# Kernel tuning notes

Measured on AMD Instinct MI355X. Metric: run time of the kernel, lower is better.

## Reference

```python
import jax, jax.numpy as jnp
import numpy as np

B, T, CM, CZ, H = 2, 512, 256, 128, 16
DH = CM // H  # 16
EPS = 1e-5


def setup_inputs() -> dict:
    root = jax.random.key(0)
    ks = jax.random.split(root, 16)
    n = lambda i, shape: jax.random.normal(ks[i], shape, dtype=jnp.float32)
    s = np.float32(1.0 / np.sqrt(CM))
    return dict(
        query=n(0, (B, T, CM)),
        key=n(1, (B, T, CM)),
        value=n(2, (B, T, CM)),
        pos_embedding=n(3, (B, 2 * T - 1, CM)),  # T2 = 2T-1 relative positions
        z=n(4, (B, T, T, CZ)),
        mask=jax.random.randint(ks[5], (B, 1, T), 0, 2) > 0,
        Wq=n(6, (CM, CM)) * s, bq=jnp.zeros((CM,), jnp.float32),
        Wk=n(7, (CM, CM)) * s, bk=jnp.zeros((CM,), jnp.float32),
        Wv=n(8, (CM, CM)) * s, bv=jnp.zeros((CM,), jnp.float32),
        Wp=n(9, (CM, CM)) * s,
        u_bias=n(10, (H, DH)) * np.float32(0.1),
        v_bias=n(11, (H, DH)) * np.float32(0.1),
        Wo=n(12, (CM, CM)) * s, bo=jnp.zeros((CM,), jnp.float32),
        ln_g=jnp.ones((CZ,), jnp.float32), ln_b=jnp.zeros((CZ,), jnp.float32),
        Wz=n(13, (CZ, H)) * np.float32(1.0 / np.sqrt(CZ)),
    )


def _relative_shift(ps):
    # ps: (B, H, T1, T2) -> Transformer-XL relative shift, keep first T2//2+1 cols
    b, h, t1, t2 = ps.shape
    padded = jnp.pad(ps, ((0, 0), (0, 0), (0, 0), (1, 0)))  # (b,h,t1,t2+1)
    padded = padded.reshape(b, h, t2 + 1, t1)
    shifted = padded[:, :, 1:, :].reshape(b, h, t1, t2)
    return shifted[..., : t2 // 2 + 1]


def reference(query, key, value, pos_embedding, z, mask,
              Wq, bq, Wk, bk, Wv, bv, Wp, u_bias, v_bias, Wo, bo,
              ln_g, ln_b, Wz):
    b = query.shape[0]
    q = (query @ Wq.T + bq).reshape(b, -1, H, DH)          # (b,T,H,dh)
    k = (key @ Wk.T + bk).reshape(b, -1, H, DH)
    v = (value @ Wv.T + bv).reshape(b, -1, H, DH)
    p = (pos_embedding @ Wp.T).reshape(b, -1, H, DH)       # (b,2T-1,H,dh)

    content = jnp.einsum('bihd,bjhd->bhij', q + u_bias, k)     # (b,H,T,T)
    pos = jnp.einsum('bihd,bjhd->bhij', q + v_bias, p)         # (b,H,T,2T-1)
    pos = _relative_shift(pos)                                  # (b,H,T,T)

    # z bias: LayerNorm over c_z then project to heads (chunking in torch is a no-op math-wise)
    mu = jnp.mean(z, axis=-1, keepdims=True)
    var = jnp.var(z, axis=-1, keepdims=True)
    zn = (z - mu) * jax.lax.rsqrt(var + EPS) * ln_g + ln_b
    z_bias = jnp.einsum('bijc,ch->bhij', zn, Wz)                # (b,H,T,T)

    score = (content + pos) / np.float32(np.sqrt(DH)) + z_bias
    score = jnp.where(mask[:, None, :, :], jnp.float32(-10000.0), score)
    attn = jax.nn.softmax(score, axis=-1)  # dropout is identity in eval

    ctx = jnp.einsum('bhij,bjhd->bihd', attn, v).reshape(b, -1, CM)
    return ctx @ Wo.T + bo
```

## Files before the change

### kernel.cpp

```cpp
#include <hip/hip_runtime.h>
#include <hip/hip_bf16.h>

typedef __attribute__((ext_vector_type(8))) short short8;
typedef __attribute__((ext_vector_type(4))) short short4v;
typedef __attribute__((ext_vector_type(4))) float f32x4;

#define LD4(dst, v4) { dst[0]=(v4).x; dst[1]=(v4).y; dst[2]=(v4).z; dst[3]=(v4).w; }

static __device__ __forceinline__ short f2bf(float f) {
    union { float f; unsigned u; } v; v.f = f;
    unsigned r = (v.u + 0x7FFFu + ((v.u >> 16) & 1u)) >> 16;
    return (short)r;
}
static __device__ __forceinline__ float bf2f(short s) {
    union { unsigned u; float f; } v; v.u = ((unsigned)(unsigned short)s) << 16;
    return v.f;
}
static __device__ __forceinline__ unsigned cvt_pk_bf16(float lo, float hi) {
    unsigned r;
    asm volatile("v_cvt_pk_bf16_f32 %0, %1, %2" : "=v"(r) : "v"(lo), "v"(hi));
    return r;
}

static __device__ __forceinline__ void proj_tile(
    const float* __restrict__ X, const float* __restrict__ W,
    const float* __restrict__ bias, float* __restrict__ Yf,
    short* __restrict__ Yb, int M, int base, float* xs)
{
    int rt = base >> 1, ct = base & 1;
    int t = threadIdx.x;
    int row_base = rt * 32;
    {
        int r = t >> 3, k0 = (t & 7) * 32;
        int row = row_base + r;
        if (row < M) {
            const float* xp = X + (size_t)row * 256 + k0;
            #pragma unroll
            for (int q = 0; q < 8; ++q) {
                float4 v = *(const float4*)(xp + q * 4);
                xs[(k0 + q * 4 + 0) * 36 + r] = v.x;
                xs[(k0 + q * 4 + 1) * 36 + r] = v.y;
                xs[(k0 + q * 4 + 2) * 36 + r] = v.z;
                xs[(k0 + q * 4 + 3) * 36 + r] = v.w;
            }
        } else {
            #pragma unroll
            for (int q = 0; q < 32; ++q) xs[(k0 + q) * 36 + r] = 0.f;
        }
    }
    __syncthreads();
    int c_base = ct * 128 + (t & 31) * 4;
    int r_base = (t >> 5) * 4;
    float acc[4][4];
    #pragma unroll
    for (int a = 0; a < 4; ++a)
        #pragma unroll
        for (int b = 0; b < 4; ++b) acc[a][b] = 0.f;
    for (int k = 0; k < 256; k += 4) {
        float w0[4], w1[4], w2[4], w3[4];
        { float4 v = *(const float4*)(W + (size_t)(c_base + 0) * 256 + k); LD4(w0, v); }
        { float4 v = *(const float4*)(W + (size_t)(c_base + 1) * 256 + k); LD4(w1, v); }
        { float4 v = *(const float4*)(W + (size_t)(c_base + 2) * 256 + k); LD4(w2, v); }
        { float4 v = *(const float4*)(W + (size_t)(c_base + 3) * 256 + k); LD4(w3, v); }
        #pragma unroll
        for (int kk = 0; kk < 4; ++kk) {
            float xl[4];
            float4 xv = *(const float4*)(&xs[(k + kk) * 36 + r_base]);
            LD4(xl, xv);
            #pragma unroll
            for (int ri = 0; ri < 4; ++ri) {
                acc[ri][0] += xl[ri] * w0[kk];
                acc[ri][1] += xl[ri] * w1[kk];
                acc[ri][2] += xl[ri] * w2[kk];
                acc[ri][3] += xl[ri] * w3[kk];
            }
        }
    }
    #pragma unroll
    for (int ri = 0; ri < 4; ++ri) {
        int row = row_base + r_base + ri;
        if (row < M) {
            float o0 = acc[ri][0] + (bias ? bias[c_base + 0] : 0.f);
            float o1 = acc[ri][1] + (bias ? bias[c_base + 1] : 0.f);
            float o2 = acc[ri][2] + (bias ? bias[c_base + 2] : 0.f);
            float o3 = acc[ri][3] + (bias ? bias[c_base + 3] : 0.f);
            if (Yb) {
                short4v o; o[0] = f2bf(o0); o[1] = f2bf(o1); o[2] = f2bf(o2); o[3] = f2bf(o3);
                *(short4v*)(Yb + (size_t)row * 256 + c_base) = o;
            } else {
                float4 o; o.x = o0; o.y = o1; o.z = o2; o.w = o3;
                *(float4*)(Yf + (size_t)row * 256 + c_base) = o;
            }
        }
    }
}

__global__ void k_proj(const float* __restrict__ query, const float* __restrict__ key,
                       const float* __restrict__ value, const float* __restrict__ pos,
                       const float* __restrict__ Wq, const float* __restrict__ bq,
                       const float* __restrict__ Wk, const float* __restrict__ bk,
                       const float* __restrict__ Wv, const float* __restrict__ bv,
                       const float* __restrict__ Wp,
                       const float* __restrict__ ln_g, const float* __restrict__ ln_b,
                       const float* __restrict__ Wz, const int* __restrict__ mask,
                       float* __restrict__ qb, short* __restrict__ kbf,
                       short* __restrict__ vbf, short* __restrict__ pbf,
                       short* __restrict__ wzp, float* __restrict__ Ah, float* __restrict__ Ch,
                       int* __restrict__ idx, int* __restrict__ cnt)
{
    __shared__ float xs[256 * 36];
    int bx = blockIdx.x;
    if (bx == 320) {
        int lane = threadIdx.x & 63, wave = threadIdx.x >> 6;
        if (wave == 0) {
            for (int b = 0; b < 2; ++b) {
                int* idxb = idx + b * 512;
                #pragma unroll
                for (int q = 0; q < 8; ++q) idxb[q * 64 + lane] = -1;
                int total = 0;
                for (int q = 0; q < 8; ++q) {
                    int j = q * 64 + lane;
                    int u = (mask[b * 512 + j] == 0) ? 1 : 0;
                    unsigned long long bal = __ballot(u);
                    int p = total + __popcll(bal & ((1ull << lane) - 1ull));
                    if (u) idxb[p] = j;
                    total += (int)__popcll(bal);
                }
                if (total == 0) {
                    for (int q = 0; q < 8; ++q) idxb[q * 64 + lane] = q * 64 + lane;
                    total = 512;
                }
                if (lane == 0) cnt[b] = total;
            }
        } else if (wave == 1) {
            for (int id = lane; id < 2048; id += 64) {
                int m = id >> 9, rem = id & 511, l = rem >> 3, ii = rem & 7;
                int c = m * 32 + ((l >> 4) << 3) + ii, h = l & 15;
                wzp[id] = f2bf(ln_g[c] * Wz[c * 16 + h]);
            }
        } else if (wave == 2) {
            int h = lane & 15, part = lane >> 4;
            float a = 0.f, c = 0.f;
            #pragma unroll 4
            for (int cc = part * 32; cc < part * 32 + 32; ++cc) {
                float wv = Wz[cc * 16 + h];
                a += ln_g[cc] * wv;
                c += ln_b[cc] * wv;
            }
            a += __shfl_xor(a, 16); a += __shfl_xor(a, 32);
            c += __shfl_xor(c, 16); c += __shfl_xor(c, 32);
            if (part == 0) { Ah[h] = a; Ch[h] = c; }
        }
        return;
    }
    if (bx < 64)       proj_tile(query, Wq, bq, qb, nullptr, 1024, bx, xs);
    else if (bx < 128) proj_tile(key,   Wk, bk, nullptr, kbf, 1024, bx - 64, xs);
    else if (bx < 192) proj_tile(value, Wv, bv, nullptr, vbf, 1024, bx - 128, xs);
    else               proj_tile(pos,   Wp, nullptr, nullptr, pbf, 2046, bx - 192, xs);
}

__global__ void __launch_bounds__(256, 4) k_z(
    const float* __restrict__ z, const short* __restrict__ wzp,
    const float* __restrict__ Ah, const float* __restrict__ Ch,
    const int* __restrict__ idx, const int* __restrict__ cnt,
    const short* __restrict__ kbf, const short* __restrict__ vbf,
    short* __restrict__ kbfC, short* __restrict__ vbTC, short* __restrict__ zacc)
{
    __shared__ short ldsb[8448];
    int bx = blockIdx.x;
    const short8 z8v = {0,0,0,0,0,0,0,0};
    if (bx < 32) {
        short* st = ldsb;
        int b = bx >> 4, jn0 = (bx & 15) * 32;
        int t = threadIdx.x;
        int r = t >> 3, cc = (t & 7) * 32;
        int jn = jn0 + r;
        int jv = idx[b * 512 + jn];
        {
            short* dst = kbfC + ((size_t)b * 512 + jn) * 256 + cc;
            if (jv >= 0) {
                const short* src = kbf + ((size_t)b * 512 + jv) * 256 + cc;
                #pragma unroll
                for (int q = 0; q < 4; ++q) *(short8*)(dst + q * 8) = *(const short8*)(src + q * 8);
            } else {
                #pragma unroll
                for (int q = 0; q < 4; ++q) *(short8*)(dst + q * 8) = z8v;
            }
        }
        {
            if (jv >= 0) {
                const short* src = vbf + ((size_t)b * 512 + jv) * 256 + cc;
                #pragma unroll
                for (int q = 0; q < 4; ++q) *(short8*)(&st[r * 264 + cc + q * 8]) = *(const short8*)(src + q * 8);
            } else {
                #pragma unroll
                for (int q = 0; q < 4; ++q) *(short8*)(&st[r * 264 + cc + q * 8]) = z8v;
            }
            __syncthreads();
            int c = t;
            short tmp[32];
            #pragma unroll
            for (int q = 0; q < 32; ++q) tmp[q] = st[q * 264 + c];
            short* dst = vbTC + ((size_t)b * 256 + c) * 512 + jn0;
            #pragma unroll
            for (int q = 0; q < 4; ++q) *(short8*)(dst + q * 8) = *(const short8*)(&tmp[q * 8]);
        }
        return;
    }
    int wave = threadIdx.x >> 6, lane = threadIdx.x & 63;
    int w = (bx - 32) * 4 + wave;
    int bi = w >> 5, tl = w & 31;
    int b = bi >> 9;
    int np = (min(cnt[b], 512) + 31) & ~31;
    if (tl * 16 >= np) return;
    short* zs = ldsb + wave * 2112;
    const int* idxr = idx + b * 512 + tl * 16;
    const float* zb_ = z + (size_t)bi * 65536;
    int l5 = lane >> 5, l31 = lane & 31;
    int idxv = idxr[lane & 15];
    #pragma unroll
    for (int m = 0; m < 8; ++m) {
        int r = 2 * m + l5;
        int jv = __shfl(idxv, r);
        int jr = (jv < 0) ? 0 : jv;
        float4 v = *(const float4*)(zb_ + (size_t)jr * 128 + l31 * 4);
        uint2 pk;
        pk.x = cvt_pk_bf16(v.x, v.y);
        pk.y = cvt_pk_bf16(v.z, v.w);
        *(uint2*)(&zs[r * 132 + l31 * 4]) = pk;
    }
    int h = lane & 15, g = lane >> 4;
    short8 wz[4];
    #pragma unroll
    for (int m = 0; m < 4; ++m) wz[m] = *(const short8*)(wzp + m * 512 + lane * 8);
    short8 af[4];
    float sum = 0.f, sq = 0.f;
    #pragma unroll
    for (int m = 0; m < 4; ++m) {
        short4v a0 = *(const short4v*)(&zs[h * 132 + g * 8 + m * 32]);
        short4v a1 = *(const short4v*)(&zs[h * 132 + g * 8 + m * 32 + 4]);
        short8 s8;
        s8[0] = a0[0]; s8[1] = a0[1]; s8[2] = a0[2]; s8[3] = a0[3];
        s8[4] = a1[0]; s8[5] = a1[1]; s8[6] = a1[2]; s8[7] = a1[3];
        af[m] = s8;
        #pragma unroll
        for (int ii = 0; ii < 8; ++ii) {
            float x = bf2f(s8[ii]);
            sum += x;
            sq = fmaf(x, x, sq);
        }
    }
    sum += __shfl_xor(sum, 16); sum += __shfl_xor(sum, 32);
    sq  += __shfl_xor(sq, 16);  sq  += __shfl_xor(sq, 32);
    float mu = sum * (1.f / 128.f);
    float rs = rsqrtf(sq * (1.f / 128.f) - mu * mu + 1e-5f);
    f32x4 acc = {0.f, 0.f, 0.f, 0.f};
    #pragma unroll
    for (int m = 0; m < 4; ++m)
        acc = __builtin_amdgcn_mfma_f32_16x16x32_bf16(af[m], wz[m], acc, 0, 0, 0);
    float ah = Ah[h], ch = Ch[h];
    short4v o;
    #pragma unroll
    for (int reg = 0; reg < 4; ++reg) {
        int orow = g * 4 + reg;
        float mo = __shfl(mu, orow);
        float ro = __shfl(rs, orow);
        o[reg] = f2bf(ro * (acc[reg] - mo * ah) + ch);
    }
    *(short4v*)(zacc + ((size_t)bi * 16 + h) * 512 + tl * 16 + g * 4) = o;
}

__global__ void __launch_bounds__(256, 4) k_attn4(
    const float* __restrict__ qb, const short* __restrict__ kbfC, const short* __restrict__ pbf,
    const short* __restrict__ zacc,
    const float* __restrict__ u_bias, const float* __restrict__ v_bias,
    const int* __restrict__ idx, const int* __restrict__ cnt,
    const short* __restrict__ vbTC,
    const float* __restrict__ Wo, const float* __restrict__ bo, float* __restrict__ out)
{
    __shared__ short wT[16 * 520];
    __shared__ float redm[64], reds[64];
    __shared__ float ctx_lds[256];
    const short8 zero8 = {0, 0, 0, 0, 0, 0, 0, 0};

    int bi = blockIdx.x;
    int b = bi >> 9, i = bi & 511;
    int t = threadIdx.x;
    int lane = t & 63, wave = t >> 6;
    int h = lane & 15, g = lane >> 4;
    int np = (min(cnt[b], 512) + 31) & ~31;
    int nt16 = np >> 4;

    bool act = ((h & 1) == (g >> 1));
    int m_act = act ? (h >> 1) : 8;
    short8 qu8 = zero8, qv8 = zero8;
    {
        int c0q = h * 16 + (g & 1) * 8;
        const float* qp = qb + (size_t)bi * 256 + c0q;
        #pragma unroll
        for (int ii = 0; ii < 8; ++ii) {
            float qv_ = qp[ii];
            qu8[ii] = f2bf(0.25f * (qv_ + u_bias[c0q + ii]));
            qv8[ii] = f2bf(0.25f * (qv_ + v_bias[c0q + ii]));
        }
        if (!act) { qu8 = zero8; qv8 = zero8; }
    }

    f32x4 sc[8];
    float mloc = -3.0e38f;
    #pragma unroll
    for (int q = 0; q < 8; ++q) {
        int tl = wave + q * 4;
        if (tl < nt16) {
            int jn = tl * 16 + h;
            int jvh = idx[b * 512 + jn];
            int jrp = 511 + ((jvh < 0) ? 0 : jvh) - i;
            const short* kr = kbfC + ((size_t)b * 512 + jn) * 256 + g * 8;
            const short* pr = pbf + ((size_t)b * 1023 + jrp) * 256 + g * 8;
            f32x4 acp = {0.f, 0.f, 0.f, 0.f};
            #pragma unroll
            for (int m = 0; m < 8; ++m) {
                short8 ka = *(const short8*)(kr + m * 32);
                short8 pa = *(const short8*)(pr + m * 32);
                short8 bu = (m == m_act) ? qu8 : zero8;
                short8 bv = (m == m_act) ? qv8 : zero8;
                acp = __builtin_amdgcn_mfma_f32_16x16x32_bf16(ka, bu, acp, 0, 0, 0);
                acp = __builtin_amdgcn_mfma_f32_16x16x32_bf16(pa, bv, acp, 0, 0, 0);
            }
            short4v za = *(const short4v*)(zacc + ((size_t)bi * 16 + h) * 512 + tl * 16 + g * 4);
            int4 jv4 = *(const int4*)(idx + b * 512 + tl * 16 + g * 4);
            int jj4[4]; jj4[0] = jv4.x; jj4[1] = jv4.y; jj4[2] = jv4.z; jj4[3] = jv4.w;
            #pragma unroll
            for (int reg = 0; reg < 4; ++reg) {
                float s = acp[reg] + bf2f(za[reg]);
                s = (jj4[reg] < 0) ? -3.0e38f : s;
                sc[q][reg] = s;
                mloc = fmaxf(mloc, s);
            }
        }
    }

    mloc = fmaxf(mloc, __shfl_xor(mloc, 16));
    mloc = fmaxf(mloc, __shfl_xor(mloc, 32));
    redm[wave * 16 + h] = mloc;
    __syncthreads();
    float mg = fmaxf(fmaxf(redm[h], redm[16 + h]), fmaxf(redm[32 + h], redm[48 + h]));
    float ssum = 0.f;
    #pragma unroll
    for (int q = 0; q < 8; ++q) {
        int tl = wave + q * 4;
        if (tl < nt16) {
            #pragma unroll
            for (int reg = 0; reg < 4; ++reg) {
                float e = __expf(sc[q][reg] - mg);
                sc[q][reg] = e;
                ssum += e;
            }
        }
    }
    ssum += __shfl_xor(ssum, 16); ssum += __shfl_xor(ssum, 32);
    reds[wave * 16 + h] = ssum;
    __syncthreads();
    float sg = reds[h] + reds[16 + h] + reds[32 + h] + reds[48 + h];
    float inv = 1.f / sg;
    #pragma unroll
    for (int q = 0; q < 8; ++q) {
        int tl = wave + q * 4;
        if (tl < nt16) {
            short4v w4;
            #pragma unroll
            for (int reg = 0; reg < 4; ++reg) w4[reg] = f2bf(sc[q][reg] * inv);
            *(short4v*)(&wT[h * 520 + tl * 16 + g * 4]) = w4;
        }
    }
    __syncthreads();

    #pragma unroll
    for (int q = 0; q < 4; ++q) {
        int hp = wave * 4 + q;
        int c0 = hp * 16;
        const short* vrow = vbTC + ((size_t)b * 256 + c0 + h) * 512;
        f32x4 a0 = {0.f, 0.f, 0.f, 0.f};
        for (int jn0 = 0; jn0 < np; jn0 += 32) {
            short8 wA = *(const short8*)(&wT[hp * 520 + jn0 + g * 8]);
            short8 vB = *(const short8*)(vrow + jn0 + g * 8);
            a0 = __builtin_amdgcn_mfma_f32_16x16x32_bf16(wA, vB, a0, 0, 0, 0);
        }
        if (g == 0) ctx_lds[c0 + h] = a0[0];
    }
    __syncthreads();

    {
        float acc = bo[t];
        const float* wrow = Wo + (size_t)t * 256;
        #pragma unroll 4
        for (int k = 0; k < 256; k += 8) {
            float4 w0 = *(const float4*)(wrow + k);
            float4 w1 = *(const float4*)(wrow + k + 4);
            acc += ctx_lds[k + 0] * w0.x + ctx_lds[k + 1] * w0.y
                 + ctx_lds[k + 2] * w0.z + ctx_lds[k + 3] * w0.w
                 + ctx_lds[k + 4] * w1.x + ctx_lds[k + 5] * w1.y
                 + ctx_lds[k + 6] * w1.z + ctx_lds[k + 7] * w1.w;
        }
        out[(size_t)bi * 256 + t] = acc;
    }
}

extern "C" void kernel_launch(void* const* d_in, const int* in_sizes, int n_in,
                              void* d_out, int out_size, void* d_ws, size_t ws_size,
                              hipStream_t stream) {
    const float* query = (const float*)d_in[0];
    const float* key   = (const float*)d_in[1];
    const float* value = (const float*)d_in[2];
    const float* pos   = (const float*)d_in[3];
    const float* z     = (const float*)d_in[4];
    const int*   mask  = (const int*)d_in[5];
    const float* Wq = (const float*)d_in[6];
    const float* bq = (const float*)d_in[7];
    const float* Wk = (const float*)d_in[8];
    const float* bk = (const float*)d_in[9];
    const float* Wv = (const float*)d_in[10];
    const float* bv = (const float*)d_in[11];
    const float* Wp = (const float*)d_in[12];
    const float* u_bias = (const float*)d_in[13];
    const float* v_bias = (const float*)d_in[14];
    const float* Wo = (const float*)d_in[15];
    const float* bo = (const float*)d_in[16];
    const float* ln_g = (const float*)d_in[17];
    const float* ln_b = (const float*)d_in[18];
    const float* Wz = (const float*)d_in[19];

    char* ws = (char*)d_ws;
    float* qb   = (float*)(ws + 0);
    short* kbf  = (short*)(ws + (1u << 20));
    short* vbf  = (short*)(ws + 1572864u);
    short* pbf  = (short*)(ws + (2u << 20));
    short* wzp  = (short*)(ws + (3u << 20));
    float* Ah   = (float*)(ws + (3u << 20) + 4096);
    float* Ch   = (float*)(ws + (3u << 20) + 4160);
    int*   idx  = (int*)(ws + (3u << 20) + 8192);
    int*   cnt  = (int*)(ws + (3u << 20) + 16384);
    short* kbfC = (short*)(ws + (4u << 20));
    short* vbTC = (short*)(ws + 4718592u);
    short* zacc = (short*)(ws + (5u << 20));

    hipLaunchKernelGGL(k_proj, dim3(321), dim3(256), 0, stream,
                       query, key, value, pos, Wq, bq, Wk, bk, Wv, bv, Wp,
                       ln_g, ln_b, Wz, mask,
                       qb, kbf, vbf, pbf, wzp, Ah, Ch, idx, cnt);
    hipLaunchKernelGGL(k_z, dim3(8224), dim3(256), 0, stream,
                       z, wzp, Ah, Ch, idx, cnt, kbf, vbf, kbfC, vbTC, zacc);
    hipLaunchKernelGGL(k_attn4, dim3(1024), dim3(256), 0, stream,
                       qb, kbfC, pbf, zacc, u_bias, v_bias, idx, cnt, vbTC,
                       Wo, bo, (float*)d_out);
}
```

Before: 183.9 us.

## Fuse projection, z-bias and attention kernels into one persistent grid-barrier megakernel

Replaces the three separate launches (projection, z LayerNorm/gather, attention) with one persistent kernel of 1024 blocks. The stages are separated by software grid barriers built on atomic counters, which a small init kernel resets. It also adds a first stage that transposes Wq/Wk/Wv/Wp/Wo into workspace so the projection and output GEMVs read weights with coalesced row access, and the projection is retiled into 16-row tiles. The aim is to remove inter-kernel launch gaps and tails and to improve weight access. The cost is extra barrier and transpose work and a dependence on all 1024 blocks being co-resident, with a spin timeout that could silently break correctness.

```diff
diff --git a/kernel.cpp b/kernel.cpp
--- a/kernel.cpp
+++ b/kernel.cpp
@@ -5,7 +5,7 @@
 typedef __attribute__((ext_vector_type(4))) short short4v;
 typedef __attribute__((ext_vector_type(4))) float f32x4;
 
-#define LD4(dst, v4) { dst[0]=(v4).x; dst[1]=(v4).y; dst[2]=(v4).z; dst[3]=(v4).w; }
+#define NBLK 1024
 
 static __device__ __forceinline__ short f2bf(float f) {
     union { float f; unsigned u; } v; v.f = f;
@@ -22,96 +22,75 @@
     return r;
 }
 
-static __device__ __forceinline__ void proj_tile(
-    const float* __restrict__ X, const float* __restrict__ W,
-    const float* __restrict__ bias, float* __restrict__ Yf,
-    short* __restrict__ Yb, int M, int base, float* xs)
-{
-    int rt = base >> 1, ct = base & 1;
-    int t = threadIdx.x;
-    int row_base = rt * 32;
-    {
-        int r = t >> 3, k0 = (t & 7) * 32;
-        int row = row_base + r;
-        if (row < M) {
-            const float* xp = X + (size_t)row * 256 + k0;
-            #pragma unroll
-            for (int q = 0; q < 8; ++q) {
-                float4 v = *(const float4*)(xp + q * 4);
-                xs[(k0 + q * 4 + 0) * 36 + r] = v.x;
-                xs[(k0 + q * 4 + 1) * 36 + r] = v.y;
-                xs[(k0 + q * 4 + 2) * 36 + r] = v.z;
-                xs[(k0 + q * 4 + 3) * 36 + r] = v.w;
-            }
+__global__ void k_init(int* bar) { if (threadIdx.x < 16) bar[threadIdx.x] = 0; }
+
+static __device__ __forceinline__ void grid_barrier(int* bar, int idx) {
+    __syncthreads();
+    if (threadIdx.x == 0) {
+        __threadfence();
+        int old = __hip_atomic_fetch_add(&bar[idx * 2], 1, __ATOMIC_ACQ_REL, __HIP_MEMORY_SCOPE_AGENT);
+        if (old == NBLK - 1) {
+            __hip_atomic_store(&bar[idx * 2 + 1], 1, __ATOMIC_RELEASE, __HIP_MEMORY_SCOPE_AGENT);
         } else {
-            #pragma unroll
-            for (int q = 0; q < 32; ++q) xs[(k0 + q) * 36 + r] = 0.f;
-        }
+            int spins = 0;
+            while (__hip_atomic_load(&bar[idx * 2 + 1], __ATOMIC_ACQUIRE, __HIP_MEMORY_SCOPE_AGENT) == 0) {
+                __builtin_amdgcn_s_sleep(2);
+                if (++spins > (1 << 22)) break;
+            }
+        }
+        __threadfence();
     }
     __syncthreads();
-    int c_base = ct * 128 + (t & 31) * 4;
-    int r_base = (t >> 5) * 4;
-    float acc[4][4];
-    #pragma unroll
-    for (int a = 0; a < 4; ++a)
-        #pragma unroll
-        for (int b = 0; b < 4; ++b) acc[a][b] = 0.f;
-    for (int k = 0; k < 256; k += 4) {
-        float w0[4], w1[4], w2[4], w3[4];
-        { float4 v = *(const float4*)(W + (size_t)(c_base + 0) * 256 + k); LD4(w0, v); }
-        { float4 v = *(const float4*)(W + (size_t)(c_base + 1) * 256 + k); LD4(w1, v); }
-        { float4 v = *(const float4*)(W + (size_t)(c_base + 2) * 256 + k); LD4(w2, v); }
-        { float4 v = *(const float4*)(W + (size_t)(c_base + 3) * 256 + k); LD4(w3, v); }
-        #pragma unroll
-        for (int kk = 0; kk < 4; ++kk) {
-            float xl[4];
-            float4 xv = *(const float4*)(&xs[(k + kk) * 36 + r_base]);
-            LD4(xl, xv);
-            #pragma unroll
-            for (int ri = 0; ri < 4; ++ri) {
-                acc[ri][0] += xl[ri] * w0[kk];
-                acc[ri][1] += xl[ri] * w1[kk];
-                acc[ri][2] += xl[ri] * w2[kk];
-                acc[ri][3] += xl[ri] * w3[kk];
-            }
-        }
-    }
-    #pragma unroll
-    for (int ri = 0; ri < 4; ++ri) {
-        int row = row_base + r_base + ri;
-        if (row < M) {
-            float o0 = acc[ri][0] + (bias ? bias[c_base + 0] : 0.f);
-            float o1 = acc[ri][1] + (bias ? bias[c_base + 1] : 0.f);
-            float o2 = acc[ri][2] + (bias ? bias[c_base + 2] : 0.f);
-            float o3 = acc[ri][3] + (bias ? bias[c_base + 3] : 0.f);
-            if (Yb) {
-                short4v o; o[0] = f2bf(o0); o[1] = f2bf(o1); o[2] = f2bf(o2); o[3] = f2bf(o3);
-                *(short4v*)(Yb + (size_t)row * 256 + c_base) = o;
-            } else {
-                float4 o; o.x = o0; o.y = o1; o.z = o2; o.w = o3;
-                *(float4*)(Yf + (size_t)row * 256 + c_base) = o;
-            }
-        }
-    }
-}
-
-__global__ void k_proj(const float* __restrict__ query, const float* __restrict__ key,
-                       const float* __restrict__ value, const float* __restrict__ pos,
-                       const float* __restrict__ Wq, const float* __restrict__ bq,
-                       const float* __restrict__ Wk, const float* __restrict__ bk,
-                       const float* __restrict__ Wv, const float* __restrict__ bv,
-                       const float* __restrict__ Wp,
-                       const float* __restrict__ ln_g, const float* __restrict__ ln_b,
-                       const float* __restrict__ Wz, const int* __restrict__ mask,
-                       float* __restrict__ qb, short* __restrict__ kbf,
-                       short* __restrict__ vbf, short* __restrict__ pbf,
-                       short* __restrict__ wzp, float* __restrict__ Ah, float* __restrict__ Ch,
-                       int* __restrict__ idx, int* __restrict__ cnt)
+}
+
+__global__ void __launch_bounds__(256, 4) k_mega(
+    const float* __restrict__ query, const float* __restrict__ key,
+    const float* __restrict__ value, const float* __restrict__ pos,
+    const float* __restrict__ z, const int* __restrict__ mask,
+    const float* __restrict__ Wq, const float* __restrict__ bq,
+    const float* __restrict__ Wk, const float* __restrict__ bk,
+    const float* __restrict__ Wv, const float* __restrict__ bv,
+    const float* __restrict__ Wp, const float* __restrict__ u_bias,
+    const float* __restrict__ v_bias, const float* __restrict__ Wo,
+    const float* __restrict__ bo, const float* __restrict__ ln_g,
+    const float* __restrict__ ln_b, const float* __restrict__ Wz,
+    float* __restrict__ qb, short* __restrict__ kbf, short* __restrict__ vbf,
+    short* __restrict__ pbf, short* __restrict__ wzp,
+    float* __restrict__ Ah, float* __restrict__ Ch,
+    int* __restrict__ idx, int* __restrict__ cnt, int* __restrict__ bar,
+    short* __restrict__ kbfC, short* __restrict__ vbTC, short* __restrict__ zacc,
+    float* __restrict__ WqT, float* __restrict__ WkT, float* __restrict__ WvT,
+    float* __restrict__ WpT, float* __restrict__ WoT, float* __restrict__ out)
 {
-    __shared__ float xs[256 * 36];
-    int bx = blockIdx.x;
-    if (bx == 320) {
-        int lane = threadIdx.x & 63, wave = threadIdx.x >> 6;
+    __shared__ __align__(16) char lds_raw[36864];
+    int bx = blockIdx.x, t = threadIdx.x;
+    int lane = t & 63, wave = t >> 6;
+
+    if (bx < 80) {
+        int mat = bx >> 4, tile = bx & 15, rt = tile >> 2, ct = tile & 3;
+        const float* src = (mat == 0) ? Wq : (mat == 1) ? Wk : (mat == 2) ? Wv : (mat == 3) ? Wp : Wo;
+        float* dst = (mat == 0) ? WqT : (mat == 1) ? WkT : (mat == 2) ? WvT : (mat == 3) ? WpT : WoT;
+        float* xsf = (float*)lds_raw;
+        int r = t >> 2, c0 = (t & 3) * 16;
+        const float* sp = src + (size_t)(rt * 64 + r) * 256 + ct * 64 + c0;
+        #pragma unroll
+        for (int u = 0; u < 4; ++u) {
+            float4 v = *(const float4*)(sp + u * 4);
+            xsf[r * 69 + c0 + u * 4 + 0] = v.x; xsf[r * 69 + c0 + u * 4 + 1] = v.y;
+            xsf[r * 69 + c0 + u * 4 + 2] = v.z; xsf[r * 69 + c0 + u * 4 + 3] = v.w;
+        }
+        __syncthreads();
+        float* dp = dst + (size_t)(ct * 64 + r) * 256 + rt * 64 + c0;
+        #pragma unroll
+        for (int u = 0; u < 4; ++u) {
+            float4 o;
+            o.x = xsf[(c0 + u * 4 + 0) * 69 + r];
+            o.y = xsf[(c0 + u * 4 + 1) * 69 + r];
+            o.z = xsf[(c0 + u * 4 + 2) * 69 + r];
+            o.w = xsf[(c0 + u * 4 + 3) * 69 + r];
+            *(float4*)(dp + u * 4) = o;
+        }
+    } else if (bx == 1023) {
         if (wave == 0) {
             for (int b = 0; b < 2; ++b) {
                 int* idxb = idx + b * 512;
@@ -151,258 +130,291 @@
             c += __shfl_xor(c, 16); c += __shfl_xor(c, 32);
             if (part == 0) { Ah[h] = a; Ch[h] = c; }
         }
-        return;
     }
-    if (bx < 64)       proj_tile(query, Wq, bq, qb, nullptr, 1024, bx, xs);
-    else if (bx < 128) proj_tile(key,   Wk, bk, nullptr, kbf, 1024, bx - 64, xs);
-    else if (bx < 192) proj_tile(value, Wv, bv, nullptr, vbf, 1024, bx - 128, xs);
-    else               proj_tile(pos,   Wp, nullptr, nullptr, pbf, 2046, bx - 192, xs);
-}
-
-__global__ void __launch_bounds__(256, 4) k_z(
-    const float* __restrict__ z, const short* __restrict__ wzp,
-    const float* __restrict__ Ah, const float* __restrict__ Ch,
-    const int* __restrict__ idx, const int* __restrict__ cnt,
-    const short* __restrict__ kbf, const short* __restrict__ vbf,
-    short* __restrict__ kbfC, short* __restrict__ vbTC, short* __restrict__ zacc)
-{
-    __shared__ short ldsb[8448];
-    int bx = blockIdx.x;
-    const short8 z8v = {0,0,0,0,0,0,0,0};
-    if (bx < 32) {
-        short* st = ldsb;
-        int b = bx >> 4, jn0 = (bx & 15) * 32;
-        int t = threadIdx.x;
-        int r = t >> 3, cc = (t & 7) * 32;
-        int jn = jn0 + r;
-        int jv = idx[b * 512 + jn];
+    grid_barrier(bar, 0);
+
+    if (bx < 640) {
+        const float* X; const float* WT_; const float* bias;
+        float* Yf = nullptr; short* Yb = nullptr; int M; int tile;
+        if (bx < 128)      { X = query; WT_ = WqT; bias = bq;      Yf = qb;  M = 1024; tile = bx; }
+        else if (bx < 256) { X = key;   WT_ = WkT; bias = bk;      Yb = kbf; M = 1024; tile = bx - 128; }
+        else if (bx < 384) { X = value; WT_ = WvT; bias = bv;      Yb = vbf; M = 1024; tile = bx - 256; }
+        else               { X = pos;   WT_ = WpT; bias = nullptr; Yb = pbf; M = 2046; tile = bx - 384; }
+        float* xs = (float*)lds_raw;
+        int rt = tile >> 1, ctile = tile & 1, row_base = rt * 16;
         {
-            short* dst = kbfC + ((size_t)b * 512 + jn) * 256 + cc;
-            if (jv >= 0) {
-                const short* src = kbf + ((size_t)b * 512 + jv) * 256 + cc;
-                #pragma unroll
-                for (int q = 0; q < 4; ++q) *(short8*)(dst + q * 8) = *(const short8*)(src + q * 8);
+            int r = t & 15, kq = (t >> 4) * 16;
+            int row = row_base + r;
+            if (row < M) {
+                const float* xp = X + (size_t)row * 256 + kq;
+                #pragma unroll
+                for (int u = 0; u < 4; ++u) {
+                    float4 v = *(const float4*)(xp + u * 4);
+                    xs[(kq + u * 4 + 0) * 17 + r] = v.x;
+                    xs[(kq + u * 4 + 1) * 17 + r] = v.y;
+                    xs[(kq + u * 4 + 2) * 17 + r] = v.z;
+                    xs[(kq + u * 4 + 3) * 17 + r] = v.w;
+                }
             } else {
                 #pragma unroll
-                for (int q = 0; q < 4; ++q) *(short8*)(dst + q * 8) = z8v;
-            }
-        }
-        {
-            if (jv >= 0) {
-                const short* src = vbf + ((size_t)b * 512 + jv) * 256 + cc;
-                #pragma unroll
-                for (int q = 0; q < 4; ++q) *(short8*)(&st[r * 264 + cc + q * 8]) = *(const short8*)(src + q * 8);
-            } else {
-                #pragma unroll
-                for (int q = 0; q < 4; ++q) *(short8*)(&st[r * 264 + cc + q * 8]) = z8v;
+                for (int u = 0; u < 16; ++u) xs[(kq + u) * 17 + r] = 0.f;
+            }
+        }
+        __syncthreads();
+        int cb = ctile * 128 + (t & 31) * 4;
+        int rb = (t >> 5) * 2;
+        float acc[2][4] = {{0.f,0.f,0.f,0.f},{0.f,0.f,0.f,0.f}};
+        for (int k = 0; k < 256; ++k) {
+            float4 w = *(const float4*)(WT_ + (size_t)k * 256 + cb);
+            float x0 = xs[k * 17 + rb], x1 = xs[k * 17 + rb + 1];
+            acc[0][0] += x0 * w.x; acc[0][1] += x0 * w.y;
+            acc[0][2] += x0 * w.z; acc[0][3] += x0 * w.w;
+            acc[1][0] += x1 * w.x; acc[1][1] += x1 * w.y;
+            acc[1][2] += x1 * w.z; acc[1][3] += x1 * w.w;
+        }
+        #pragma unroll
+        for (int ri = 0; ri < 2; ++ri) {
+            int row = row_base + rb + ri;
+            if (row < M) {
+                float o0 = acc[ri][0] + (bias ? bias[cb + 0] : 0.f);
+                float o1 = acc[ri][1] + (bias ? bias[cb + 1] : 0.f);
+                float o2 = acc[ri][2] + (bias ? bias[cb + 2] : 0.f);
+                float o3 = acc[ri][3] + (bias ? bias[cb + 3] : 0.f);
+                if (Yb) {
+                    short4v o; o[0] = f2bf(o0); o[1] = f2bf(o1); o[2] = f2bf(o2); o[3] = f2bf(o3);
+                    *(short4v*)(Yb + (size_t)row * 256 + cb) = o;
+                } else {
+                    float4 o; o.x = o0; o.y = o1; o.z = o2; o.w = o3;
+                    *(float4*)(Yf + (size_t)row * 256 + cb) = o;
+                }
+            }
+        }
+    }
+    grid_barrier(bar, 1);
+
+    {
+        const short8 z8v = {0,0,0,0,0,0,0,0};
+        if (bx < 32) {
+            short* st = (short*)lds_raw;
+            int b = bx >> 4, jn0 = (bx & 15) * 32;
+            int r = t >> 3, cc = (t & 7) * 32;
+            int jn = jn0 + r;
+            int jv = idx[b * 512 + jn];
+            {
+                short* dst = kbfC + ((size_t)b * 512 + jn) * 256 + cc;
+                if (jv >= 0) {
+                    const short* src = kbf + ((size_t)b * 512 + jv) * 256 + cc;
+                    #pragma unroll
+                    for (int q = 0; q < 4; ++q) *(short8*)(dst + q * 8) = *(const short8*)(src + q * 8);
+                } else {
+                    #pragma unroll
+                    for (int q = 0; q < 4; ++q) *(short8*)(dst + q * 8) = z8v;
+                }
+            }
+            {
+                if (jv >= 0) {
+                    const short* src = vbf + ((size_t)b * 512 + jv) * 256 + cc;
+                    #pragma unroll
+                    for (int q = 0; q < 4; ++q) *(short8*)(&st[r * 264 + cc + q * 8]) = *(const short8*)(src + q * 8);
+                } else {
+                    #pragma unroll
+                    for (int q = 0; q < 4; ++q) *(short8*)(&st[r * 264 + cc + q * 8]) = z8v;
+                }
+                __syncthreads();
+                int c = t;
+                short tmp[32];
+                #pragma unroll
+                for (int q = 0; q < 32; ++q) tmp[q] = st[q * 264 + c];
+                short* dst = vbTC + ((size_t)b * 256 + c) * 512 + jn0;
+                #pragma unroll
+                for (int q = 0; q < 4; ++q) *(short8*)(dst + q * 8) = *(const short8*)(&tmp[q * 8]);
             }
             __syncthreads();
-            int c = t;
-            short tmp[32];
-            #pragma unroll
-            for (int q = 0; q < 32; ++q) tmp[q] = st[q * 264 + c];
-            short* dst = vbTC + ((size_t)b * 256 + c) * 512 + jn0;
-            #pragma unroll
-            for (int q = 0; q < 4; ++q) *(short8*)(dst + q * 8) = *(const short8*)(&tmp[q * 8]);
-        }
-        return;
-    }
-    int wave = threadIdx.x >> 6, lane = threadIdx.x & 63;
-    int w = (bx - 32) * 4 + wave;
-    int bi = w >> 5, tl = w & 31;
-    int b = bi >> 9;
-    int np = (min(cnt[b], 512) + 31) & ~31;
-    if (tl * 16 >= np) return;
-    short* zs = ldsb + wave * 2112;
-    const int* idxr = idx + b * 512 + tl * 16;
-    const float* zb_ = z + (size_t)bi * 65536;
-    int l5 = lane >> 5, l31 = lane & 31;
-    int idxv = idxr[lane & 15];
-    #pragma unroll
-    for (int m = 0; m < 8; ++m) {
-        int r = 2 * m + l5;
-        int jv = __shfl(idxv, r);
-        int jr = (jv < 0) ? 0 : jv;
-        float4 v = *(const float4*)(zb_ + (size_t)jr * 128 + l31 * 4);
-        uint2 pk;
-        pk.x = cvt_pk_bf16(v.x, v.y);
-        pk.y = cvt_pk_bf16(v.z, v.w);
-        *(uint2*)(&zs[r * 132 + l31 * 4]) = pk;
-    }
-    int h = lane & 15, g = lane >> 4;
-    short8 wz[4];
-    #pragma unroll
-    for (int m = 0; m < 4; ++m) wz[m] = *(const short8*)(wzp + m * 512 + lane * 8);
-    short8 af[4];
-    float sum = 0.f, sq = 0.f;
-    #pragma unroll
-    for (int m = 0; m < 4; ++m) {
-        short4v a0 = *(const short4v*)(&zs[h * 132 + g * 8 + m * 32]);
-        short4v a1 = *(const short4v*)(&zs[h * 132 + g * 8 + m * 32 + 4]);
-        short8 s8;
-        s8[0] = a0[0]; s8[1] = a0[1]; s8[2] = a0[2]; s8[3] = a0[3];
-        s8[4] = a1[0]; s8[5] = a1[1]; s8[6] = a1[2]; s8[7] = a1[3];
-        af[m] = s8;
-        #pragma unroll
-        for (int ii = 0; ii < 8; ++ii) {
-            float x = bf2f(s8[ii]);
-            sum += x;
-            sq = fmaf(x, x, sq);
-        }
-    }
-    sum += __shfl_xor(sum, 16); sum += __shfl_xor(sum, 32);
-    sq  += __shfl_xor(sq, 16);  sq  += __shfl_xor(sq, 32);
-    float mu = sum * (1.f / 128.f);
-    float rs = rsqrtf(sq * (1.f / 128.f) - mu * mu + 1e-5f);
-    f32x4 acc = {0.f, 0.f, 0.f, 0.f};
-    #pragma unroll
-    for (int m = 0; m < 4; ++m)
-        acc = __builtin_amdgcn_mfma_f32_16x16x32_bf16(af[m], wz[m], acc, 0, 0, 0);
-    float ah = Ah[h], ch = Ch[h];
-    short4v o;
-    #pragma unroll
-    for (int reg = 0; reg < 4; ++reg) {
-        int orow = g * 4 + reg;
-        float mo = __shfl(mu, orow);
-        float ro = __shfl(rs, orow);
-        o[reg] = f2bf(ro * (acc[reg] - mo * ah) + ch);
-    }
-    *(short4v*)(zacc + ((size_t)bi * 16 + h) * 512 + tl * 16 + g * 4) = o;
-}
-
-__global__ void __launch_bounds__(256, 4) k_attn4(
-    const float* __restrict__ qb, const short* __restrict__ kbfC, const short* __restrict__ pbf,
-    const short* __restrict__ zacc,
-    const float* __restrict__ u_bias, const float* __restrict__ v_bias,
-    const int* __restrict__ idx, const int* __restrict__ cnt,
-    const short* __restrict__ vbTC,
-    const float* __restrict__ Wo, const float* __restrict__ bo, float* __restrict__ out)
-{
-    __shared__ short wT[16 * 520];
-    __shared__ float redm[64], reds[64];
-    __shared__ float ctx_lds[256];
-    const short8 zero8 = {0, 0, 0, 0, 0, 0, 0, 0};
-
-    int bi = blockIdx.x;
-    int b = bi >> 9, i = bi & 511;
-    int t = threadIdx.x;
-    int lane = t & 63, wave = t >> 6;
-    int h = lane & 15, g = lane >> 4;
-    int np = (min(cnt[b], 512) + 31) & ~31;
-    int nt16 = np >> 4;
-
-    bool act = ((h & 1) == (g >> 1));
-    int m_act = act ? (h >> 1) : 8;
-    short8 qu8 = zero8, qv8 = zero8;
-    {
-        int c0q = h * 16 + (g & 1) * 8;
-        const float* qp = qb + (size_t)bi * 256 + c0q;
-        #pragma unroll
-        for (int ii = 0; ii < 8; ++ii) {
-            float qv_ = qp[ii];
-            qu8[ii] = f2bf(0.25f * (qv_ + u_bias[c0q + ii]));
-            qv8[ii] = f2bf(0.25f * (qv_ + v_bias[c0q + ii]));
-        }
-        if (!act) { qu8 = zero8; qv8 = zero8; }
-    }
-
-    f32x4 sc[8];
-    float mloc = -3.0e38f;
-    #pragma unroll
-    for (int q = 0; q < 8; ++q) {
-        int tl = wave + q * 4;
-        if (tl < nt16) {
-            int jn = tl * 16 + h;
-            int jvh = idx[b * 512 + jn];
-            int jrp = 511 + ((jvh < 0) ? 0 : jvh) - i;
-            const short* kr = kbfC + ((size_t)b * 512 + jn) * 256 + g * 8;
-            const short* pr = pbf + ((size_t)b * 1023 + jrp) * 256 + g * 8;
-            f32x4 acp = {0.f, 0.f, 0.f, 0.f};
+        }
+        int cnt0 = cnt[0], cnt1 = cnt[1];
+        short* zs = (short*)lds_raw + wave * 2112;
+        int h = lane & 15, g = lane >> 4;
+        short8 wz[4];
+        #pragma unroll
+        for (int m = 0; m < 4; ++m) wz[m] = *(const short8*)(wzp + m * 512 + lane * 8);
+        float ah = Ah[h], ch = Ch[h];
+        int l5 = lane >> 5, l31 = lane & 31;
+        for (int tt = 0; tt < 8; ++tt) {
+            int tid = (bx * 4 + wave) * 8 + tt;
+            int bi = tid >> 5, tl = tid & 31;
+            int b = bi >> 9;
+            int np = (min(b ? cnt1 : cnt0, 512) + 31) & ~31;
+            if (tl * 16 >= np) continue;
+            const int* idxr = idx + b * 512 + tl * 16;
+            const float* zb_ = z + (size_t)bi * 65536;
+            int idxv = idxr[lane & 15];
             #pragma unroll
             for (int m = 0; m < 8; ++m) {
-                short8 ka = *(const short8*)(kr + m * 32);
-                short8 pa = *(const short8*)(pr + m * 32);
-                short8 bu = (m == m_act) ? qu8 : zero8;
-                short8 bv = (m == m_act) ? qv8 : zero8;
-                acp = __builtin_amdgcn_mfma_f32_16x16x32_bf16(ka, bu, acp, 0, 0, 0);
-                acp = __builtin_amdgcn_mfma_f32_16x16x32_bf16(pa, bv, acp, 0, 0, 0);
-            }
-            short4v za = *(const short4v*)(zacc + ((size_t)bi * 16 + h) * 512 + tl * 16 + g * 4);
-            int4 jv4 = *(const int4*)(idx + b * 512 + tl * 16 + g * 4);
-            int jj4[4]; jj4[0] = jv4.x; jj4[1] = jv4.y; jj4[2] = jv4.z; jj4[3] = jv4.w;
+                int r = 2 * m + l5;
+                int jv = __shfl(idxv, r);
+                int jr = (jv < 0) ? 0 : jv;
+                float4 v = *(const float4*)(zb_ + (size_t)jr * 128 + l31 * 4);
+                uint2 pk;
+                pk.x = cvt_pk_bf16(v.x, v.y);
+                pk.y = cvt_pk_bf16(v.z, v.w);
+                *(uint2*)(&zs[r * 132 + l31 * 4]) = pk;
+            }
+            short8 af[4];
+            float sum = 0.f, sq = 0.f;
+            #pragma unroll
+            for (int m = 0; m < 4; ++m) {
+                short4v a0 = *(const short4v*)(&zs[h * 132 + g * 8 + m * 32]);
+                short4v a1 = *(const short4v*)(&zs[h * 132 + g * 8 + m * 32 + 4]);
+                short8 s8;
+                s8[0] = a0[0]; s8[1] = a0[1]; s8[2] = a0[2]; s8[3] = a0[3];
+                s8[4] = a1[0]; s8[5] = a1[1]; s8[6] = a1[2]; s8[7] = a1[3];
+                af[m] = s8;
+                #pragma unroll
+                for (int ii = 0; ii < 8; ++ii) {
+                    float x = bf2f(s8[ii]);
+                    sum += x;
+                    sq = fmaf(x, x, sq);
+                }
+            }
+            sum += __shfl_xor(sum, 16); sum += __shfl_xor(sum, 32);
+            sq  += __shfl_xor(sq, 16);  sq  += __shfl_xor(sq, 32);
+            float mu = sum * (1.f / 128.f);
+            float rs = rsqrtf(sq * (1.f / 128.f) - mu * mu + 1e-5f);
+            f32x4 acc = {0.f, 0.f, 0.f, 0.f};
+            #pragma unroll
+            for (int m = 0; m < 4; ++m)
+                acc = __builtin_amdgcn_mfma_f32_16x16x32_bf16(af[m], wz[m], acc, 0, 0, 0);
+            short4v o;
             #pragma unroll
             for (int reg = 0; reg < 4; ++reg) {
-                float s = acp[reg] + bf2f(za[reg]);
-                s = (jj4[reg] < 0) ? -3.0e38f : s;
-                sc[q][reg] = s;
-                mloc = fmaxf(mloc, s);
-            }
+                int orow = g * 4 + reg;
+                float mo = __shfl(mu, orow);
+                float ro = __shfl(rs, orow);
+                o[reg] = f2bf(ro * (acc[reg] - mo * ah) + ch);
+            }
+            *(short4v*)(zacc + ((size_t)bi * 16 + h) * 512 + tl * 16 + g * 4) = o;
         }
     }
-
-    mloc = fmaxf(mloc, __shfl_xor(mloc, 16));
-    mloc = fmaxf(mloc, __shfl_xor(mloc, 32));
-    redm[wave * 16 + h] = mloc;
-    __syncthreads();
-    float mg = fmaxf(fmaxf(redm[h], redm[16 + h]), fmaxf(redm[32 + h], redm[48 + h]));
-    float ssum = 0.f;
-    #pragma unroll
-    for (int q = 0; q < 8; ++q) {
-        int tl = wave + q * 4;
-        if (tl < nt16) {
+    grid_barrier(bar, 2);
+
+    {
+        short* wT   = (short*)lds_raw;
+        float* redm = (float*)(lds_raw + 16640);
+        float* reds = (float*)(lds_raw + 16896);
+        float* ctxl = (float*)(lds_raw + 17152);
+        const short8 zero8 = {0, 0, 0, 0, 0, 0, 0, 0};
+        int bi = bx;
+        int b = bi >> 9, i = bi & 511;
+        int h = lane & 15, g = lane >> 4;
+        int np = (min(cnt[b], 512) + 31) & ~31;
+        int nt16 = np >> 4;
+
+        bool act = ((h & 1) == (g >> 1));
+        int m_act = act ? (h >> 1) : 8;
+        short8 qu8 = zero8, qv8 = zero8;
+        {
+            int c0q = h * 16 + (g & 1) * 8;
+            const float* qp = qb + (size_t)bi * 256 + c0q;
             #pragma unroll
-            for (int reg = 0; reg < 4; ++reg) {
-                float e = __expf(sc[q][reg] - mg);
-                sc[q][reg] = e;
-                ssum += e;
-            }
-        }
-    }
-    ssum += __shfl_xor(ssum, 16); ssum += __shfl_xor(ssum, 32);
-    reds[wave * 16 + h] = ssum;
-    __syncthreads();
-    float sg = reds[h] + reds[16 + h] + reds[32 + h] + reds[48 + h];
-    float inv = 1.f / sg;
-    #pragma unroll
-    for (int q = 0; q < 8; ++q) {
-        int tl = wave + q * 4;
-        if (tl < nt16) {
-            short4v w4;
-            #pragma unroll
-            for (int reg = 0; reg < 4; ++reg) w4[reg] = f2bf(sc[q][reg] * inv);
-            *(short4v*)(&wT[h * 520 + tl * 16 + g * 4]) = w4;
-        }
-    }
-    __syncthreads();
-
-    #pragma unroll
-    for (int q = 0; q < 4; ++q) {
-        int hp = wave * 4 + q;
-        int c0 = hp * 16;
-        const short* vrow = vbTC + ((size_t)b * 256 + c0 + h) * 512;
-        f32x4 a0 = {0.f, 0.f, 0.f, 0.f};
-        for (int jn0 = 0; jn0 < np; jn0 += 32) {
-            short8 wA = *(const short8*)(&wT[hp * 520 + jn0 + g * 8]);
-            short8 vB = *(const short8*)(vrow + jn0 + g * 8);
-            a0 = __builtin_amdgcn_mfma_f32_16x16x32_bf16(wA, vB, a0, 0, 0, 0);
-        }
-        if (g == 0) ctx_lds[c0 + h] = a0[0];
-    }
-    __syncthreads();
-
-    {
-        float acc = bo[t];
-        const float* wrow = Wo + (size_t)t * 256;
-        #pragma unroll 4
-        for (int k = 0; k < 256; k += 8) {
-            float4 w0 = *(const float4*)(wrow + k);
-            float4 w1 = *(const float4*)(wrow + k + 4);
-            acc += ctx_lds[k + 0] * w0.x + ctx_lds[k + 1] * w0.y
-                 + ctx_lds[k + 2] * w0.z + ctx_lds[k + 3] * w0.w
-                 + ctx_lds[k + 4] * w1.x + ctx_lds[k + 5] * w1.y
-                 + ctx_lds[k + 6] * w1.z + ctx_lds[k + 7] * w1.w;
-        }
-        out[(size_t)bi * 256 + t] = acc;
+            for (int ii = 0; ii < 8; ++ii) {
+                float qv_ = qp[ii];
+                qu8[ii] = f2bf(0.25f * (qv_ + u_bias[c0q + ii]));
+                qv8[ii] = f2bf(0.25f * (qv_ + v_bias[c0q + ii]));
+            }
+            if (!act) { qu8 = zero8; qv8 = zero8; }
+        }
+
+        f32x4 sc[8];
+        float mloc = -3.0e38f;
+        #pragma unroll
+        for (int q = 0; q < 8; ++q) {
+            int tl = wave + q * 4;
+            if (tl < nt16) {
+                int jn = tl * 16 + h;
+                int jvh = idx[b * 512 + jn];
+                int jrp = 511 + ((jvh < 0) ? 0 : jvh) - i;
+                const short* kr = kbfC + ((size_t)b * 512 + jn) * 256 + g * 8;
+                const short* pr = pbf + ((size_t)b * 1023 + jrp) * 256 + g * 8;
+                f32x4 acp = {0.f, 0.f, 0.f, 0.f};
+                #pragma unroll
+                for (int m = 0; m < 8; ++m) {
+                    short8 ka = *(const short8*)(kr + m * 32);
+                    short8 pa = *(const short8*)(pr + m * 32);
+                    short8 bu = (m == m_act) ? qu8 : zero8;
+                    short8 bv = (m == m_act) ? qv8 : zero8;
+                    acp = __builtin_amdgcn_mfma_f32_16x16x32_bf16(ka, bu, acp, 0, 0, 0);
+                    acp = __builtin_amdgcn_mfma_f32_16x16x32_bf16(pa, bv, acp, 0, 0, 0);
+                }
+                short4v za = *(const short4v*)(zacc + ((size_t)bi * 16 + h) * 512 + tl * 16 + g * 4);
+                int4 jv4 = *(const int4*)(idx + b * 512 + tl * 16 + g * 4);
+                int jj4[4]; jj4[0] = jv4.x; jj4[1] = jv4.y; jj4[2] = jv4.z; jj4[3] = jv4.w;
+                #pragma unroll
+                for (int reg = 0; reg < 4; ++reg) {
+                    float s = acp[reg] + bf2f(za[reg]);
+                    s = (jj4[reg] < 0) ? -3.0e38f : s;
+                    sc[q][reg] = s;
+                    mloc = fmaxf(mloc, s);
+                }
+            }
+        }
+
+        mloc = fmaxf(mloc, __shfl_xor(mloc, 16));
+        mloc = fmaxf(mloc, __shfl_xor(mloc, 32));
+        redm[wave * 16 + h] = mloc;
+        __syncthreads();
+        float mg = fmaxf(fmaxf(redm[h], redm[16 + h]), fmaxf(redm[32 + h], redm[48 + h]));
+        float ssum = 0.f;
+        #pragma unroll
+        for (int q = 0; q < 8; ++q) {
+            int tl = wave + q * 4;
+            if (tl < nt16) {
+                #pragma unroll
+                for (int reg = 0; reg < 4; ++reg) {
+                    float e = __expf(sc[q][reg] - mg);
+                    sc[q][reg] = e;
+                    ssum += e;
+                }
+            }
+        }
+        ssum += __shfl_xor(ssum, 16); ssum += __shfl_xor(ssum, 32);
+        reds[wave * 16 + h] = ssum;
+        __syncthreads();
+        float sg = reds[h] + reds[16 + h] + reds[32 + h] + reds[48 + h];
+        float inv = 1.f / sg;
+        #pragma unroll
+        for (int q = 0; q < 8; ++q) {
+            int tl = wave + q * 4;
+            if (tl < nt16) {
+                short4v w4;
+                #pragma unroll
+                for (int reg = 0; reg < 4; ++reg) w4[reg] = f2bf(sc[q][reg] * inv);
+                *(short4v*)(&wT[h * 520 + tl * 16 + g * 4]) = w4;
+            }
+        }
+        __syncthreads();
+
+        #pragma unroll
+        for (int q = 0; q < 4; ++q) {
+            int hp = wave * 4 + q;
+            int c0 = hp * 16;
+            const short* vrow = vbTC + ((size_t)b * 256 + c0 + h) * 512;
+            f32x4 a0 = {0.f, 0.f, 0.f, 0.f};
+            for (int jn0 = 0; jn0 < np; jn0 += 32) {
+                short8 wA = *(const short8*)(&wT[hp * 520 + jn0 + g * 8]);
+                short8 vB = *(const short8*)(vrow + jn0 + g * 8);
+                a0 = __builtin_amdgcn_mfma_f32_16x16x32_bf16(wA, vB, a0, 0, 0, 0);
+            }
+            if (g == 0) ctxl[c0 + h] = a0[0];
+        }
+        __syncthreads();
+
+        {
+            float acc = bo[t];
+            #pragma unroll 8
+            for (int k = 0; k < 256; ++k)
+                acc += ctxl[k] * WoT[(size_t)k * 256 + t];
+            out[(size_t)bi * 256 + t] = acc;
+        }
     }
 }
 
@@ -440,17 +452,21 @@
     float* Ch   = (float*)(ws + (3u << 20) + 4160);
     int*   idx  = (int*)(ws + (3u << 20) + 8192);
     int*   cnt  = (int*)(ws + (3u << 20) + 16384);
+    int*   bar  = (int*)(ws + (3u << 20) + 16448);
     short* kbfC = (short*)(ws + (4u << 20));
     short* vbTC = (short*)(ws + 4718592u);
     short* zacc = (short*)(ws + (5u << 20));
-
-    hipLaunchKernelGGL(k_proj, dim3(321), dim3(256), 0, stream,
-                       query, key, value, pos, Wq, bq, Wk, bk, Wv, bv, Wp,
-                       ln_g, ln_b, Wz, mask,
-                       qb, kbf, vbf, pbf, wzp, Ah, Ch, idx, cnt);
-    hipLaunchKernelGGL(k_z, dim3(8224), dim3(256), 0, stream,
-                       z, wzp, Ah, Ch, idx, cnt, kbf, vbf, kbfC, vbTC, zacc);
-    hipLaunchKernelGGL(k_attn4, dim3(1024), dim3(256), 0, stream,
-                       qb, kbfC, pbf, zacc, u_bias, v_bias, idx, cnt, vbTC,
-                       Wo, bo, (float*)d_out);
-}
+    float* WqT  = (float*)(ws + (22u << 20));
+    float* WkT  = (float*)(ws + (22u << 20) + 262144u);
+    float* WvT  = (float*)(ws + (22u << 20) + 524288u);
+    float* WpT  = (float*)(ws + (22u << 20) + 786432u);
+    float* WoT  = (float*)(ws + (22u << 20) + 1048576u);
+
+    hipLaunchKernelGGL(k_init, dim3(1), dim3(64), 0, stream, bar);
+    hipLaunchKernelGGL(k_mega, dim3(NBLK), dim3(256), 0, stream,
+                       query, key, value, pos, z, mask,
+                       Wq, bq, Wk, bk, Wv, bv, Wp, u_bias, v_bias, Wo, bo,
+                       ln_g, ln_b, Wz,
+                       qb, kbf, vbf, pbf, wzp, Ah, Ch, idx, cnt, bar,
+                       kbfC, vbTC, zacc, WqT, WkT, WvT, WpT, WoT, (float*)d_out);
+}
```

After: 665.7 us. 3.62x slower.
